# Optimization experiments

Measured on AMD Instinct MI355X. Metric: run time of the kernel, lower is better.

## Reference

```python
import jax, jax.numpy as jnp
import numpy as np

C = 64            # irrep multiplicity (64x0e + 64x1o)
N_BASIS = 8
N_SPECIES = 5
AVG_NEIGH = 16.0
CUTOFF = 5.0
N_PATHS = 5       # (0e*Y0->0e),(0e*Y1->1o),(1o*Y0->1o),(1o.Y1->0e),(1o x Y1->1)


def setup_inputs() -> dict:
    key = jax.random.key(0)
    ks = jax.random.split(key, 16)
    N, E = 20000, 320000
    def w(k, shape, fan_in):
        return jax.random.normal(k, shape, dtype=jnp.float32) / jnp.sqrt(jnp.float32(fan_in))
    return {
        "vectors": jax.random.normal(ks[0], (E, 3), dtype=jnp.float32),
        "node_feats": jax.random.normal(ks[1], (N, 4 * C), dtype=jnp.float32),
        "node_specie": jax.random.randint(ks[2], (N,), 0, N_SPECIES),
        "senders": jax.random.randint(ks[3], (E,), 0, N),
        "receivers": jax.random.randint(ks[4], (E,), 0, N),
        # linear_up (per-irrep channel mixing)
        "W0_up": w(ks[5], (C, C), C),
        "W1_up": w(ks[6], (C, C), C),
        # radial MLP: 8 -> 64 -> 64 -> 5*C
        "Wm1": w(ks[7], (N_BASIS, 64), N_BASIS),
        "Wm2": w(ks[8], (64, 64), 64),
        "Wm3": w(ks[9], (64, N_PATHS * C), 64),
        # skip_tp: species-indexed linear to 128x0e + 64x1o
        "Ws0": w(ks[10], (N_SPECIES, C, 2 * C), C),
        "Ws1": w(ks[11], (N_SPECIES, C, C), C),
        # linear_down: messages irreps -> 128x0e + 64x1o
        "Wd0": w(ks[12], (C, 2 * C), C),
        "Wd1": w(ks[13], (C, C), C),
    }


def reference(vectors, node_feats, node_specie, senders, receivers,
              W0_up, W1_up, Wm1, Wm2, Wm3, Ws0, Ws1, Wd0, Wd1):
    N = node_feats.shape[0]
    E = vectors.shape[0]
    x0 = node_feats[:, :C]                       # [N,C]   0e scalars
    x1 = node_feats[:, C:].reshape(N, C, 3)      # [N,C,3] 1o vectors

    # linear_up then gather by senders
    u0 = x0 @ W0_up
    u1 = jnp.einsum('nci,cd->ndi', x1, W1_up)
    m0 = u0[senders]                             # [E,C]
    m1 = u1[senders]                             # [E,C,3]

    # radial basis (bessel) and edge-weight MLP
    r = jnp.linalg.norm(vectors, axis=-1, keepdims=True)   # [E,1]
    safe_r = jnp.where(r == 0.0, 1.0, r)
    Y1 = vectors / safe_r                                  # [E,3] unit direction (l=1 SH)
    n = jnp.arange(1, N_BASIS + 1, dtype=vectors.dtype)
    basis = jnp.sqrt(2.0 / CUTOFF) * jnp.sin(n * jnp.pi * r / CUTOFF) / safe_r  # [E,8]
    h = jax.nn.silu(basis @ Wm1)
    h = jax.nn.silu(h @ Wm2)
    wmix = h @ Wm3                                         # [E, 5*C]
    wmix = jnp.where(r == 0.0, 0.0, wmix)                  # zero weights at zero-length edges
    w00, w01, w10, w11d, w11c = jnp.split(wmix, N_PATHS, axis=-1)  # each [E,C]

    # per-edge equivariant tensor product (LinearSHTP, l<=1 CG paths)
    dot = jnp.einsum('eci,ei->ec', m1, Y1)                 # 1o . Y1 -> scalar
    crs = jnp.cross(m1, Y1[:, None, :])                    # 1o x Y1 -> vector
    msg0 = w00 * m0 + w11d * dot                           # [E,C]
    msg1 = (w01 * m0)[..., None] * Y1[:, None, :] \
           + w10[..., None] * m1 + w11c[..., None] * crs   # [E,C,3]

    # scatter_sum to receivers, normalize by sqrt(avg_num_neighbors)
    inv = 1.0 / jnp.sqrt(jnp.float32(AVG_NEIGH))
    a0 = jax.ops.segment_sum(msg0, receivers, num_segments=N) * inv
    a1 = jax.ops.segment_sum(msg1.reshape(E, 3 * C), receivers, num_segments=N).reshape(N, C, 3) * inv

    # linear_down to 128x0e + 64x1o (extra 0e scalars are the gates)
    d0 = a0 @ Wd0                                          # [N,2C]
    d1 = jnp.einsum('nci,cd->ndi', a1, Wd1)                # [N,C,3]

    # skip_tp: species-indexed linear on original node features
    s0 = jnp.einsum('nc,ncd->nd', x0, Ws0[node_specie])    # [N,2C]
    s1 = jnp.einsum('nci,ncd->ndi', x1, Ws1[node_specie])  # [N,C,3]

    f0 = d0 + s0
    f1 = d1 + s1

    # gate: first C scalars -> even_act(silu); next C scalars gate the 1o vectors
    scalars = jax.nn.silu(f0[:, :C])
    gates = jax.nn.silu(f0[:, C:])
    vec = f1 * gates[..., None]
    return jnp.concatenate([scalars, vec.reshape(N, 3 * C)], axis=-1)  # [N, 4C]
```

## Files before the change

kernel.cpp:

```cpp
#include <hip/hip_runtime.h>
#include <hip/hip_bf16.h>

typedef __attribute__((ext_vector_type(8))) short short8;
typedef __attribute__((ext_vector_type(4))) float f32x4;

__device__ __forceinline__ unsigned bf16u(float x) {
    unsigned u = __float_as_uint(x);
    return (u + 0x7fffu + ((u >> 16) & 1u)) >> 16;
}
__device__ __forceinline__ short bf16s(float x) { return (short)bf16u(x); }

__global__ __launch_bounds__(256) void prep_kernel(
    const float* __restrict__ Wm1, const float* __restrict__ Wm2,
    const float* __restrict__ Wm3,
    const float* __restrict__ Wd0, const float* __restrict__ Ws0,
    const float* __restrict__ Wd1, const float* __restrict__ Ws1,
    short* __restrict__ W1B, short* __restrict__ Wm2B, short* __restrict__ W3B,
    short* __restrict__ WoB, int* __restrict__ cnt, int N)
{
    const int tid = blockIdx.x * 256 + threadIdx.x;
    const int nth = gridDim.x * 256;

    for (int i = tid; i < N * 16; i += nth) cnt[i] = 0;

    for (int idx = tid; idx < 52 * 64; idx += nth) {
        int l = idx & 63, f = idx >> 6;
        int g = l >> 4, c = l & 15;
        short8 v;
        if (f < 4) {
            #pragma unroll
            for (int i = 0; i < 8; ++i)
                v[i] = (g == 0) ? bf16s(Wm1[(size_t)i * 64 + f * 16 + c]) : (short)0;
            *(short8*)(W1B + (size_t)f * 512 + l * 8) = v;
        } else if (f < 12) {
            int f2 = f - 4, t = f2 >> 1, kh = f2 & 1;
            #pragma unroll
            for (int i = 0; i < 8; ++i)
                v[i] = bf16s(Wm2[(size_t)(kh * 32 + g * 8 + i) * 64 + t * 16 + c]);
            *(short8*)(Wm2B + (size_t)f2 * 512 + l * 8) = v;
        } else {
            int f3 = f - 12, t = f3 >> 1, kh = f3 & 1;
            #pragma unroll
            for (int i = 0; i < 8; ++i)
                v[i] = bf16s(Wm3[(size_t)(kh * 32 + g * 8 + i) * 320 + t * 16 + c]);
            *(short8*)(W3B + (size_t)f3 * 512 + l * 8) = v;
        }
    }

    for (int idx = tid; idx < 144 * 64; idx += nth) {
        int l = idx & 63, f = idx >> 6;
        int g = l >> 4, c = l & 15;
        short8 v;
        if (f < 16) {
            int t = f >> 1, kh = f & 1;
            #pragma unroll
            for (int i = 0; i < 8; ++i)
                v[i] = bf16s(Wd0[(size_t)(kh * 32 + g * 8 + i) * 128 + t * 16 + c]);
        } else if (f < 96) {
            int s = (f - 16) >> 4, r = (f - 16) & 15, t = r >> 1, kh = r & 1;
            #pragma unroll
            for (int i = 0; i < 8; ++i)
                v[i] = bf16s(Ws0[((size_t)s * 64 + kh * 32 + g * 8 + i) * 128 + t * 16 + c]);
        } else if (f < 104) {
            int r = f - 96, t = r >> 1, kh = r & 1;
            #pragma unroll
            for (int i = 0; i < 8; ++i)
                v[i] = bf16s(Wd1[(size_t)(kh * 32 + g * 8 + i) * 64 + t * 16 + c]);
        } else {
            int s = (f - 104) >> 3, r = (f - 104) & 7, t = r >> 1, kh = r & 1;
            #pragma unroll
            for (int i = 0; i < 8; ++i)
                v[i] = bf16s(Ws1[((size_t)s * 64 + kh * 32 + g * 8 + i) * 64 + t * 16 + c]);
        }
        *(short8*)(WoB + (size_t)f * 512 + l * 8) = v;
    }
}

__global__ __launch_bounds__(256) void rank_kernel(
    const int* __restrict__ receivers, int* __restrict__ cnt,
    int* __restrict__ rank, int E)
{
    int i = blockIdx.x * 256 + threadIdx.x;
    int stride = gridDim.x * 256;
    for (; i < E; i += stride)
        rank[i] = atomicAdd(&cnt[receivers[i] << 4], 1);
}

__global__ __launch_bounds__(256) void scan1_kernel(
    const int* __restrict__ cnt, int* __restrict__ offs,
    int* __restrict__ part, int N)
{
    __shared__ int a_[256], b_[256];
    const int b = blockIdx.x, t = threadIdx.x;
    const int base = b * 1024 + t * 4;
    int v[4];
    #pragma unroll
    for (int k = 0; k < 4; ++k)
        v[k] = (base + k < N) ? cnt[(size_t)(base + k) << 4] : 0;
    int sum = v[0] + v[1] + v[2] + v[3];
    a_[t] = sum;
    __syncthreads();
    int* src = a_; int* dst = b_;
    for (int off = 1; off < 256; off <<= 1) {
        dst[t] = src[t] + ((t >= off) ? src[t - off] : 0);
        __syncthreads();
        int* tmp = src; src = dst; dst = tmp;
    }
    int excl = src[t] - sum;
    if (t == 0) part[b] = src[255];
    int run = excl;
    #pragma unroll
    for (int k = 0; k < 4; ++k) {
        if (base + k < N) offs[base + k] = run;
        run += v[k];
    }
}

__global__ __launch_bounds__(256) void scan23_kernel(
    int* __restrict__ offs, const int* __restrict__ part, int nblk, int N)
{
    __shared__ int base_s, total_s;
    const int b = blockIdx.x, t = threadIdx.x;
    if (t == 0) {
        int s = 0, tot = 0;
        for (int i = 0; i < nblk; ++i) {
            if (i < b) s += part[i];
            tot += part[i];
        }
        base_s = s; total_s = tot;
    }
    __syncthreads();
    const int add = base_s;
    const int base = b * 1024 + t * 4;
    #pragma unroll
    for (int k = 0; k < 4; ++k) {
        int i = base + k;
        if (i < N) offs[i] += add;
    }
    if (b == 0 && t == 0) offs[N] = total_s;
}

__global__ __launch_bounds__(256) void fpnu_kernel(
    const float* __restrict__ vectors, const int* __restrict__ senders,
    const int* __restrict__ receivers, const int* __restrict__ offs,
    const int* __restrict__ rank,
    uint4* __restrict__ epackA, float4* __restrict__ epackB,
    const float* __restrict__ node_feats, const float* __restrict__ W0_up,
    const float* __restrict__ W1_up, uint2* __restrict__ ubf,
    short* __restrict__ xpk, int E, int N, int FPB)
{
    __shared__ float lnf[4][256];
    if (blockIdx.x < FPB) {
        int i = blockIdx.x * 256 + threadIdx.x;
        int stride = FPB * 256;
        for (; i < E; i += stride) {
            int pos = offs[receivers[i]] + rank[i];
            float vx = vectors[3 * (size_t)i + 0];
            float vy = vectors[3 * (size_t)i + 1];
            float vz = vectors[3 * (size_t)i + 2];
            float r = sqrtf(vx * vx + vy * vy + vz * vz);
            float ir = (r != 0.f) ? 1.f / r : 0.f;
            float ang = r * 0.6283185307179586f;
            float s1, c1;
            __sincosf(ang, &s1, &c1);
            float tc = 2.f * c1;
            float sb = s1, sp = 0.f;
            float coef = 0.6324555320336759f * ir;
            unsigned bw[4];
            #pragma unroll
            for (int h = 0; h < 4; ++h) {
                unsigned lo = bf16u(sb * coef);
                float nx = tc * sb - sp; sp = sb; sb = nx;
                unsigned hi = bf16u(sb * coef);
                nx = tc * sb - sp; sp = sb; sb = nx;
                bw[h] = lo | (hi << 16);
            }
            epackA[pos] = make_uint4(bw[0], bw[1], bw[2], bw[3]);
            epackB[pos] = make_float4(vx * ir, vy * ir, vz * ir,
                                      __int_as_float(senders[i]));
        }
    } else {
        const int wv = threadIdx.x >> 6;
        const int d  = threadIdx.x & 63;
        int nb = (blockIdx.x - FPB) * 4 + wv;
        if (nb >= N) return;

        float4 v4 = *(const float4*)(node_feats + (size_t)nb * 256 + d * 4);
        *(float4*)&lnf[wv][d * 4] = v4;

        float a0 = 0.f, ax = 0.f, ay = 0.f, az = 0.f;
        #pragma unroll 8
        for (int cc = 0; cc < 64; ++cc) {
            float w0 = W0_up[cc * 64 + d];
            float w1 = W1_up[cc * 64 + d];
            float x0v = lnf[wv][cc];
            float xxv = lnf[wv][64 + cc * 3 + 0];
            float xyv = lnf[wv][64 + cc * 3 + 1];
            float xzv = lnf[wv][64 + cc * 3 + 2];
            a0 += x0v * w0;
            ax += xxv * w1;
            ay += xyv * w1;
            az += xzv * w1;
        }
        ubf[(size_t)nb * 64 + d] = make_uint2(bf16u(a0) | (bf16u(ax) << 16),
                                              bf16u(ay) | (bf16u(az) << 16));
        short* xp = xpk + (size_t)nb * 256;
        xp[d]       = bf16s(lnf[wv][d]);
        xp[64 + d]  = bf16s(lnf[wv][64 + d * 3 + 0]);
        xp[128 + d] = bf16s(lnf[wv][64 + d * 3 + 1]);
        xp[192 + d] = bf16s(lnf[wv][64 + d * 3 + 2]);
    }
}

__global__ __launch_bounds__(256) void mlp_kernel(
    const uint4* __restrict__ epackA,
    const short* __restrict__ W1B, const short* __restrict__ Wm2B,
    const short* __restrict__ W3B, unsigned short* __restrict__ wmix,
    int P, int nwaves)
{
    __shared__ __align__(16) short ldsW3[40 * 512];
    __shared__ __align__(16) short ldsH[4][1024];

    {
        const short8* src = (const short8*)W3B;
        short8* dst = (short8*)ldsW3;
        for (int i = threadIdx.x; i < 2560; i += 256) dst[i] = src[i];
    }
    __syncthreads();

    const int lane = threadIdx.x & 63;
    const int wv   = threadIdx.x >> 6;
    const int gw   = blockIdx.x * 4 + wv;
    const int c = lane & 15, g = lane >> 4;
    const int nwin = (P + 15) >> 4;

    for (int w = gw; w < nwin; w += nwaves) {
        const int p0 = w << 4;

        short8 basisA = {0, 0, 0, 0, 0, 0, 0, 0};
        if (lane < 16) {
            uint4 ba = epackA[p0 + lane];
            union { uint4 u4v; short8 s8; } cv;
            cv.u4v = ba;
            basisA = cv.s8;
        }

        #pragma unroll
        for (int t = 0; t < 4; ++t) {
            f32x4 h = {0.f, 0.f, 0.f, 0.f};
            short8 bf = *(const short8*)(W1B + (size_t)t * 512 + lane * 8);
            h = __builtin_amdgcn_mfma_f32_16x16x32_bf16(basisA, bf, h, 0, 0, 0);
            #pragma unroll
            for (int i = 0; i < 4; ++i) {
                float x = h[i];
                float h1 = x / (1.f + __expf(-x));
                int row = 4 * g + i;
                ldsH[wv][row * 64 + ((16 * t + c) ^ ((row & 7) << 3))] = bf16s(h1);
            }
        }
        short8 h1f0 = *(const short8*)&ldsH[wv][c * 64 + ((g * 8) ^ ((c & 7) << 3))];
        short8 h1f1 = *(const short8*)&ldsH[wv][c * 64 + ((32 + g * 8) ^ ((c & 7) << 3))];

        #pragma unroll
        for (int t = 0; t < 4; ++t) {
            f32x4 h = {0.f, 0.f, 0.f, 0.f};
            short8 b0 = *(const short8*)(Wm2B + (size_t)(t * 2) * 512 + lane * 8);
            short8 b1 = *(const short8*)(Wm2B + (size_t)(t * 2 + 1) * 512 + lane * 8);
            h = __builtin_amdgcn_mfma_f32_16x16x32_bf16(h1f0, b0, h, 0, 0, 0);
            h = __builtin_amdgcn_mfma_f32_16x16x32_bf16(h1f1, b1, h, 0, 0, 0);
            #pragma unroll
            for (int i = 0; i < 4; ++i) {
                float x = h[i];
                float h2 = x / (1.f + __expf(-x));
                int row = 4 * g + i;
                ldsH[wv][row * 64 + ((16 * t + c) ^ ((row & 7) << 3))] = bf16s(h2);
            }
        }
        short8 h2f0 = *(const short8*)&ldsH[wv][c * 64 + ((g * 8) ^ ((c & 7) << 3))];
        short8 h2f1 = *(const short8*)&ldsH[wv][c * 64 + ((32 + g * 8) ^ ((c & 7) << 3))];

        size_t rowOfs[4];
        bool ok[4];
        #pragma unroll
        for (int i = 0; i < 4; ++i) {
            int row = p0 + 4 * g + i;
            ok[i] = (row < P);
            rowOfs[i] = (size_t)row * 320;
        }
        #pragma unroll
        for (int t = 0; t < 20; ++t) {
            f32x4 wq = {0.f, 0.f, 0.f, 0.f};
            short8 b0 = *(const short8*)(ldsW3 + (size_t)(t * 2) * 512 + lane * 8);
            short8 b1 = *(const short8*)(ldsW3 + (size_t)(t * 2 + 1) * 512 + lane * 8);
            wq = __builtin_amdgcn_mfma_f32_16x16x32_bf16(h2f0, b0, wq, 0, 0, 0);
            wq = __builtin_amdgcn_mfma_f32_16x16x32_bf16(h2f1, b1, wq, 0, 0, 0);
            const int col = (t >> 2) * 64 + (t & 3) * 16 + c;
            #pragma unroll
            for (int i = 0; i < 4; ++i)
                if (ok[i]) wmix[rowOfs[i] + col] = (unsigned short)bf16u(wq[i]);
        }
    }
}

__global__ __launch_bounds__(256) void gather_kernel(
    const float4* __restrict__ epackB, const int* __restrict__ offs,
    const uint2* __restrict__ ubf, const unsigned short* __restrict__ wmix,
    float* __restrict__ acc, int N)
{
    const int lane = threadIdx.x & 63;
    const int n = blockIdx.x * 4 + (threadIdx.x >> 6);
    if (n >= N) return;

    const int beg = offs[n], end = offs[n + 1];
    float a0 = 0.f, a1x = 0.f, a1y = 0.f, a1z = 0.f;

    #pragma unroll 2
    for (int pos = beg; pos < end; ++pos) {
        float4 mb = epackB[pos];
        int snd = __float_as_int(mb.w);
        uint2 mu = ubf[(size_t)snd * 64 + lane];
        const unsigned short* wr = wmix + (size_t)pos * 320;
        float w00  = __uint_as_float((unsigned)wr[lane]        << 16);
        float w01  = __uint_as_float((unsigned)wr[64 + lane]   << 16);
        float w10  = __uint_as_float((unsigned)wr[128 + lane]  << 16);
        float w11d = __uint_as_float((unsigned)wr[192 + lane]  << 16);
        float w11c = __uint_as_float((unsigned)wr[256 + lane]  << 16);
        float m0  = __uint_as_float(mu.x << 16);
        float m1x = __uint_as_float(mu.x & 0xffff0000u);
        float m1y = __uint_as_float(mu.y << 16);
        float m1z = __uint_as_float(mu.y & 0xffff0000u);

        float dotv = m1x * mb.x + m1y * mb.y + m1z * mb.z;
        a0 += w00 * m0 + w11d * dotv;
        float wm = w01 * m0;
        a1x += wm * mb.x + w10 * m1x + w11c * (m1y * mb.z - m1z * mb.y);
        a1y += wm * mb.y + w10 * m1y + w11c * (m1z * mb.x - m1x * mb.z);
        a1z += wm * mb.z + w10 * m1z + w11c * (m1x * mb.y - m1y * mb.x);
    }

    float* ar = acc + (size_t)n * 256;
    ar[lane]       = a0;
    ar[64 + lane]  = a1x;
    ar[128 + lane] = a1y;
    ar[192 + lane] = a1z;
}

__global__ __launch_bounds__(256) void edge_kernel(
    const uint4* __restrict__ epackA, const float4* __restrict__ epackB,
    const int* __restrict__ offs, const uint2* __restrict__ ubf,
    const short* __restrict__ W1B, const short* __restrict__ Wm2B,
    const short* __restrict__ W3B, float* __restrict__ acc,
    int N, int nwaves)
{
    __shared__ __align__(16) short ldsW3[40 * 512];
    __shared__ __align__(16) short ldsH[4][1024];
    __shared__ __align__(16) float ldsMeta[4][16][4];

    {
        const short8* src = (const short8*)W3B;
        short8* dst = (short8*)ldsW3;
        for (int i = threadIdx.x; i < 2560; i += 256) dst[i] = src[i];
    }
    __syncthreads();

    const int lane = threadIdx.x & 63;
    const int wv   = threadIdx.x >> 6;
    const int gw   = blockIdx.x * 4 + wv;
    const int c = lane & 15, g = lane >> 4;

    for (int n = gw; n < N; n += nwaves) {
        float a0q[4]  = {0.f, 0.f, 0.f, 0.f};
        float a1xq[4] = {0.f, 0.f, 0.f, 0.f};
        float a1yq[4] = {0.f, 0.f, 0.f, 0.f};
        float a1zq[4] = {0.f, 0.f, 0.f, 0.f};
        const int beg = offs[n], end = offs[n + 1];

        for (int p0 = beg; p0 < end; p0 += 16) {
            const int m = end - p0;
            short8 basisA = {0, 0, 0, 0, 0, 0, 0, 0};
            if (lane < 16) {
                uint4 ba = epackA[p0 + lane];
                float4 mb = epackB[p0 + lane];
                if (lane >= m) {
                    ba = make_uint4(0u, 0u, 0u, 0u);
                    mb = make_float4(0.f, 0.f, 0.f, __int_as_float(0));
                }
                union { uint4 u4v; short8 s8; } cv;
                cv.u4v = ba;
                basisA = cv.s8;
                *(float4*)&ldsMeta[wv][lane][0] = mb;
            }
            float Yx[4], Yy[4], Yz[4];
            int snd[4];
            #pragma unroll
            for (int i = 0; i < 4; ++i) {
                float4 mt = *(const float4*)&ldsMeta[wv][4 * g + i][0];
                Yx[i] = mt.x; Yy[i] = mt.y; Yz[i] = mt.z;
                snd[i] = __float_as_int(mt.w);
            }

#define PFETCH(Q, MV)                                                       \
            _Pragma("unroll")                                               \
            for (int i = 0; i < 4; ++i)                                     \
                MV[i] = ubf[(size_t)snd[i] * 64 + 16 * (Q) + c];

#define COMPQ(Q, MV)                                                        \
        {                                                                   \
            float M0[4], M1X[4], M1Y[4], M1Z[4];                            \
            _Pragma("unroll")                                               \
            for (int i = 0; i < 4; ++i) {                                   \
                M0[i]  = __uint_as_float(MV[i].x << 16);                    \
                M1X[i] = __uint_as_float(MV[i].x & 0xffff0000u);            \
                M1Y[i] = __uint_as_float(MV[i].y << 16);                    \
                M1Z[i] = __uint_as_float(MV[i].y & 0xffff0000u);            \
            }                                                               \
            _Pragma("unroll")                                               \
            for (int p = 0; p < 5; ++p) {                                   \
                const int t = 4 * p + (Q);                                  \
                f32x4 w = {0.f, 0.f, 0.f, 0.f};                             \
                short8 b0 = *(const short8*)(ldsW3 + (size_t)(t * 2) * 512 + lane * 8);     \
                short8 b1 = *(const short8*)(ldsW3 + (size_t)(t * 2 + 1) * 512 + lane * 8); \
                w = __builtin_amdgcn_mfma_f32_16x16x32_bf16(h2f0, b0, w, 0, 0, 0);          \
                w = __builtin_amdgcn_mfma_f32_16x16x32_bf16(h2f1, b1, w, 0, 0, 0);          \
                _Pragma("unroll")                                           \
                for (int i = 0; i < 4; ++i) {                               \
                    float wv_ = w[i];                                       \
                    if (p == 0) {                                           \
                        a0q[Q] += wv_ * M0[i];                              \
                    } else if (p == 1) {                                    \
                        float tt = wv_ * M0[i];                             \
                        a1xq[Q] += tt * Yx[i];                              \
                        a1yq[Q] += tt * Yy[i];                              \
                        a1zq[Q] += tt * Yz[i];                              \
                    } else if (p == 2) {                                    \
                        a1xq[Q] += wv_ * M1X[i];                            \
                        a1yq[Q] += wv_ * M1Y[i];                            \
                        a1zq[Q] += wv_ * M1Z[i];                            \
                    } else if (p == 3) {                                    \
                        a0q[Q] += wv_ * (M1X[i] * Yx[i] + M1Y[i] * Yy[i] + M1Z[i] * Yz[i]); \
                    } else {                                                \
                        a1xq[Q] += wv_ * (M1Y[i] * Yz[i] - M1Z[i] * Yy[i]); \
                        a1yq[Q] += wv_ * (M1Z[i] * Yx[i] - M1X[i] * Yz[i]); \
                        a1zq[Q] += wv_ * (M1X[i] * Yy[i] - M1Y[i] * Yx[i]); \
                    }                                                       \
                }                                                           \
            }                                                               \
        }

            uint2 mA[4], mB[4];
            PFETCH(0, mA);
            PFETCH(1, mB);
            __builtin_amdgcn_sched_barrier(0);

            #pragma unroll
            for (int t = 0; t < 4; ++t) {
                f32x4 h = {0.f, 0.f, 0.f, 0.f};
                short8 bf = *(const short8*)(W1B + (size_t)t * 512 + lane * 8);
                h = __builtin_amdgcn_mfma_f32_16x16x32_bf16(basisA, bf, h, 0, 0, 0);
                #pragma unroll
                for (int i = 0; i < 4; ++i) {
                    float x = h[i];
                    float h1 = x / (1.f + __expf(-x));
                    int row = 4 * g + i;
                    ldsH[wv][row * 64 + ((16 * t + c) ^ ((row & 7) << 3))] = bf16s(h1);
                }
            }
            short8 h1f0 = *(const short8*)&ldsH[wv][c * 64 + ((g * 8) ^ ((c & 7) << 3))];
            short8 h1f1 = *(const short8*)&ldsH[wv][c * 64 + ((32 + g * 8) ^ ((c & 7) << 3))];

            #pragma unroll
            for (int t = 0; t < 4; ++t) {
                f32x4 h = {0.f, 0.f, 0.f, 0.f};
                short8 b0 = *(const short8*)(Wm2B + (size_t)(t * 2) * 512 + lane * 8);
                short8 b1 = *(const short8*)(Wm2B + (size_t)(t * 2 + 1) * 512 + lane * 8);
                h = __builtin_amdgcn_mfma_f32_16x16x32_bf16(h1f0, b0, h, 0, 0, 0);
                h = __builtin_amdgcn_mfma_f32_16x16x32_bf16(h1f1, b1, h, 0, 0, 0);
                #pragma unroll
                for (int i = 0; i < 4; ++i) {
                    float x = h[i];
                    float h2 = x / (1.f + __expf(-x));
                    int row = 4 * g + i;
                    ldsH[wv][row * 64 + ((16 * t + c) ^ ((row & 7) << 3))] = bf16s(h2);
                }
            }
            short8 h2f0 = *(const short8*)&ldsH[wv][c * 64 + ((g * 8) ^ ((c & 7) << 3))];
            short8 h2f1 = *(const short8*)&ldsH[wv][c * 64 + ((32 + g * 8) ^ ((c & 7) << 3))];

            COMPQ(0, mA);
            __builtin_amdgcn_sched_barrier(0);
            PFETCH(2, mA);
            COMPQ(1, mB);
            __builtin_amdgcn_sched_barrier(0);
            PFETCH(3, mB);
            COMPQ(2, mA);
            __builtin_amdgcn_sched_barrier(0);
            COMPQ(3, mB);
#undef PFETCH
#undef COMPQ
        }

        #pragma unroll
        for (int q = 0; q < 4; ++q) {
            a0q[q]  += __shfl_xor(a0q[q], 16);  a0q[q]  += __shfl_xor(a0q[q], 32);
            a1xq[q] += __shfl_xor(a1xq[q], 16); a1xq[q] += __shfl_xor(a1xq[q], 32);
            a1yq[q] += __shfl_xor(a1yq[q], 16); a1yq[q] += __shfl_xor(a1yq[q], 32);
            a1zq[q] += __shfl_xor(a1zq[q], 16); a1zq[q] += __shfl_xor(a1zq[q], 32);
        }
        if (lane < 16) {
            float* ar = acc + (size_t)n * 256;
            #pragma unroll
            for (int q = 0; q < 4; ++q) {
                ar[16 * q + lane]       = a0q[q];
                ar[64 + 16 * q + lane]  = a1xq[q];
                ar[128 + 16 * q + lane] = a1yq[q];
                ar[192 + 16 * q + lane] = a1zq[q];
            }
        }
    }
}

__global__ __launch_bounds__(256) void node_out_kernel(
    const float* __restrict__ acc, const short* __restrict__ xpk,
    const int* __restrict__ node_specie, const short* __restrict__ WoB,
    float* __restrict__ out, int N)
{
    __shared__ float ldsOut[4][16][256];
    const int lane = threadIdx.x & 63;
    const int wv   = threadIdx.x >> 6;
    const int c = lane & 15, g = lane >> 4;
    const int n0 = (blockIdx.x * 4 + wv) * 16;
    if (n0 >= N) return;

    const int nc = min(n0 + c, N - 1);
    const int sp_c = node_specie[nc];
    const short8 z8 = {0, 0, 0, 0, 0, 0, 0, 0};

    short8 x0f[2], a0hi[2], a0lo[2];
    #pragma unroll
    for (int kh = 0; kh < 2; ++kh) {
        x0f[kh] = *(const short8*)&xpk[(size_t)nc * 256 + kh * 32 + g * 8];
        const float* ap = acc + (size_t)nc * 256 + kh * 32 + g * 8;
        #pragma unroll
        for (int i = 0; i < 8; ++i) {
            float v = 0.25f * ap[i];
            unsigned h = bf16u(v);
            a0hi[kh][i] = (short)h;
            a0lo[kh][i] = (short)bf16u(v - __uint_as_float(h << 16));
        }
    }

    f32x4 w0[8];
    #pragma unroll
    for (int t = 0; t < 8; ++t) w0[t] = (f32x4){0.f, 0.f, 0.f, 0.f};
    #pragma unroll
    for (int t = 0; t < 8; ++t)
        #pragma unroll
        for (int kh = 0; kh < 2; ++kh) {
            short8 b = *(const short8*)(WoB + (size_t)(t * 2 + kh) * 512 + lane * 8);
            w0[t] = __builtin_amdgcn_mfma_f32_16x16x32_bf16(a0hi[kh], b, w0[t], 0, 0, 0);
            w0[t] = __builtin_amdgcn_mfma_f32_16x16x32_bf16(a0lo[kh], b, w0[t], 0, 0, 0);
        }
    #pragma unroll
    for (int s = 0; s < 5; ++s) {
        if (!__any(sp_c == s)) continue;
        short8 mk0 = (sp_c == s) ? x0f[0] : z8;
        short8 mk1 = (sp_c == s) ? x0f[1] : z8;
        #pragma unroll
        for (int t = 0; t < 8; ++t) {
            short8 b0 = *(const short8*)(WoB + (size_t)(16 + s * 16 + t * 2) * 512 + lane * 8);
            short8 b1 = *(const short8*)(WoB + (size_t)(16 + s * 16 + t * 2 + 1) * 512 + lane * 8);
            w0[t] = __builtin_amdgcn_mfma_f32_16x16x32_bf16(mk0, b0, w0[t], 0, 0, 0);
            w0[t] = __builtin_amdgcn_mfma_f32_16x16x32_bf16(mk1, b1, w0[t], 0, 0, 0);
        }
    }
    float gate[4][4];
    #pragma unroll
    for (int t = 0; t < 8; ++t)
        #pragma unroll
        for (int i = 0; i < 4; ++i) {
            float x = w0[t][i];
            float sv = x / (1.f + __expf(-x));
            if (t < 4) ldsOut[wv][4 * g + i][16 * t + c] = sv;
            else       gate[t - 4][i] = sv;
        }

    short8 x1f[3][2], a1hi[3][2], a1lo[3][2];
    #pragma unroll
    for (int j = 0; j < 3; ++j)
        #pragma unroll
        for (int kh = 0; kh < 2; ++kh) {
            x1f[j][kh] = *(const short8*)&xpk[(size_t)nc * 256 + (1 + j) * 64 + kh * 32 + g * 8];
            const float* ap = acc + (size_t)nc * 256 + 64 + 64 * j + kh * 32 + g * 8;
            #pragma unroll
            for (int i = 0; i < 8; ++i) {
                float v = 0.25f * ap[i];
                unsigned h = bf16u(v);
                a1hi[j][kh][i] = (short)h;
                a1lo[j][kh][i] = (short)bf16u(v - __uint_as_float(h << 16));
            }
        }

    f32x4 w1[3][4];
    #pragma unroll
    for (int j = 0; j < 3; ++j)
        #pragma unroll
        for (int t = 0; t < 4; ++t) w1[j][t] = (f32x4){0.f, 0.f, 0.f, 0.f};
    #pragma unroll
    for (int t = 0; t < 4; ++t)
        #pragma unroll
        for (int kh = 0; kh < 2; ++kh) {
            short8 b = *(const short8*)(WoB + (size_t)(96 + t * 2 + kh) * 512 + lane * 8);
            #pragma unroll
            for (int j = 0; j < 3; ++j) {
                w1[j][t] = __builtin_amdgcn_mfma_f32_16x16x32_bf16(a1hi[j][kh], b, w1[j][t], 0, 0, 0);
                w1[j][t] = __builtin_amdgcn_mfma_f32_16x16x32_bf16(a1lo[j][kh], b, w1[j][t], 0, 0, 0);
            }
        }
    #pragma unroll
    for (int s = 0; s < 5; ++s) {
        if (!__any(sp_c == s)) continue;
        short8 m1[3][2];
        #pragma unroll
        for (int j = 0; j < 3; ++j) {
            m1[j][0] = (sp_c == s) ? x1f[j][0] : z8;
            m1[j][1] = (sp_c == s) ? x1f[j][1] : z8;
        }
        #pragma unroll
        for (int t = 0; t < 4; ++t)
            #pragma unroll
            for (int kh = 0; kh < 2; ++kh) {
                short8 b = *(const short8*)(WoB + (size_t)(104 + s * 8 + t * 2 + kh) * 512 + lane * 8);
                #pragma unroll
                for (int j = 0; j < 3; ++j)
                    w1[j][t] = __builtin_amdgcn_mfma_f32_16x16x32_bf16(m1[j][kh], b, w1[j][t], 0, 0, 0);
            }
    }
    #pragma unroll
    for (int j = 0; j < 3; ++j)
        #pragma unroll
        for (int t = 0; t < 4; ++t)
            #pragma unroll
            for (int i = 0; i < 4; ++i)
                ldsOut[wv][4 * g + i][64 + (16 * t + c) * 3 + j] = w1[j][t][i] * gate[t][i];

    #pragma unroll 4
    for (int r = 0; r < 16; ++r) {
        int nn = n0 + r;
        if (nn < N)
            *(float4*)&out[(size_t)nn * 256 + lane * 4] =
                *(const float4*)&ldsOut[wv][r][lane * 4];
    }
}

extern "C" void kernel_launch(void* const* d_in, const int* in_sizes, int n_in,
                              void* d_out, int out_size, void* d_ws, size_t ws_size,
                              hipStream_t stream) {
    const float* vectors     = (const float*)d_in[0];
    const float* node_feats  = (const float*)d_in[1];
    const int*   node_specie = (const int*)d_in[2];
    const int*   senders     = (const int*)d_in[3];
    const int*   receivers   = (const int*)d_in[4];
    const float* W0_up       = (const float*)d_in[5];
    const float* W1_up       = (const float*)d_in[6];
    const float* Wm1         = (const float*)d_in[7];
    const float* Wm2         = (const float*)d_in[8];
    const float* Wm3         = (const float*)d_in[9];
    const float* Ws0         = (const float*)d_in[10];
    const float* Ws1         = (const float*)d_in[11];
    const float* Wd0         = (const float*)d_in[12];
    const float* Wd1         = (const float*)d_in[13];
    float* out = (float*)d_out;

    int E = in_sizes[0] / 3;
    int N = in_sizes[1] / 256;
    int nblk = (N + 1023) / 1024;

    char* wp = (char*)d_ws;
    uint2* ubf     = (uint2*)wp;                wp += (size_t)N * 64 * 8;
    float* acc     = (float*)wp;                wp += (size_t)N * 256 * 4;
    short* xpk     = (short*)wp;                wp += (size_t)N * 256 * 2;
    uint4* epackA  = (uint4*)wp;                wp += (size_t)(E + 16) * 16;
    float4* epackB = (float4*)wp;               wp += (size_t)(E + 16) * 16;
    unsigned short* wmix = (unsigned short*)wp;
    size_t wmix_bytes = (size_t)(E + 16) * 320 * 2;
    size_t base_used = (size_t)(wp - (char*)d_ws);
    size_t other_bytes = (4 + 8 + 40 + 144) * 512 * 2
                       + (size_t)N * 16 * 4
                       + (size_t)(N + 1) * 4
                       + (size_t)E * 4
                       + (size_t)(nblk + 1) * 4 + 256;
    bool use_split = (base_used + wmix_bytes + other_bytes) <= ws_size;
    if (use_split) wp += wmix_bytes;

    short* W1B    = (short*)wp;                 wp += 4 * 512 * 2;
    short* Wm2B   = (short*)wp;                 wp += 8 * 512 * 2;
    short* W3B    = (short*)wp;                 wp += 40 * 512 * 2;
    short* WoB    = (short*)wp;                 wp += 144 * 512 * 2;
    int*   cnt    = (int*)wp;                   wp += (size_t)N * 16 * 4;
    int*   offs   = (int*)wp;                   wp += (size_t)(N + 1) * 4;
    int*   rank   = (int*)wp;                   wp += (size_t)E * 4;
    int*   part   = (int*)wp;                   wp += (size_t)(nblk + 1) * 4;

    prep_kernel<<<80, 256, 0, stream>>>(
        Wm1, Wm2, Wm3, Wd0, Ws0, Wd1, Ws1, W1B, Wm2B, W3B, WoB, cnt, N);
    rank_kernel<<<1024, 256, 0, stream>>>(receivers, cnt, rank, E);
    scan1_kernel<<<nblk, 256, 0, stream>>>(cnt, offs, part, N);
    scan23_kernel<<<nblk, 256, 0, stream>>>(offs, part, nblk, N);
    const int FPB = 1024;
    fpnu_kernel<<<FPB + (N + 3) / 4, 256, 0, stream>>>(
        vectors, senders, receivers, offs, rank, epackA, epackB,
        node_feats, W0_up, W1_up, ubf, xpk, E, N, FPB);

    if (use_split) {
        mlp_kernel<<<768, 256, 0, stream>>>(
            epackA, W1B, Wm2B, W3B, wmix, E, 768 * 4);
        gather_kernel<<<(N + 3) / 4, 256, 0, stream>>>(
            epackB, offs, ubf, wmix, acc, N);
    } else {
        edge_kernel<<<512, 256, 0, stream>>>(
            epackA, epackB, offs, ubf, W1B, Wm2B, W3B, acc, N, 512 * 4);
    }

    int ngroups = (N + 15) / 16;
    node_out_kernel<<<(ngroups + 3) / 4, 256, 0, stream>>>(
        acc, xpk, node_specie, WoB, out, N);
}
```

Before: 195.7 us.

## Store edge weights in MFMA-native tiled layout with vectorized 8-byte stores and loads

The weight-MLP kernel now writes each wave's 16-edge by 320-column result tile directly in the MFMA fragment order, as one 4-element bf16 vector store per lane per tile, with no per-row bounds checks or scattered 2-byte stores. The gather kernel reads that tiled layout in groups of four edges, loading five 8-byte vectors per group instead of five 2-byte loads per edge, and masks edges outside the node's range. This trades scattered narrow global writes and reads for wide coalesced ones. It requires the wmix buffer to be padded to a multiple of 16 edges, and boundary edges at group edges are loaded and then discarded.

```diff
diff --git a/kernel.cpp b/kernel.cpp
--- a/kernel.cpp
+++ b/kernel.cpp
@@ -3,6 +3,7 @@
 
 typedef __attribute__((ext_vector_type(8))) short short8;
 typedef __attribute__((ext_vector_type(4))) float f32x4;
+typedef __attribute__((ext_vector_type(4))) unsigned short us4v;
 
 __device__ __forceinline__ unsigned bf16u(float x) {
     unsigned u = __float_as_uint(x);
@@ -279,14 +280,7 @@
         short8 h2f0 = *(const short8*)&ldsH[wv][c * 64 + ((g * 8) ^ ((c & 7) << 3))];
         short8 h2f1 = *(const short8*)&ldsH[wv][c * 64 + ((32 + g * 8) ^ ((c & 7) << 3))];
 
-        size_t rowOfs[4];
-        bool ok[4];
-        #pragma unroll
-        for (int i = 0; i < 4; ++i) {
-            int row = p0 + 4 * g + i;
-            ok[i] = (row < P);
-            rowOfs[i] = (size_t)row * 320;
-        }
+        unsigned short* wbase = wmix + (size_t)w * 5120 + lane * 4;
         #pragma unroll
         for (int t = 0; t < 20; ++t) {
             f32x4 wq = {0.f, 0.f, 0.f, 0.f};
@@ -294,10 +288,10 @@
             short8 b1 = *(const short8*)(ldsW3 + (size_t)(t * 2 + 1) * 512 + lane * 8);
             wq = __builtin_amdgcn_mfma_f32_16x16x32_bf16(h2f0, b0, wq, 0, 0, 0);
             wq = __builtin_amdgcn_mfma_f32_16x16x32_bf16(h2f1, b1, wq, 0, 0, 0);
-            const int col = (t >> 2) * 64 + (t & 3) * 16 + c;
-            #pragma unroll
-            for (int i = 0; i < 4; ++i)
-                if (ok[i]) wmix[rowOfs[i] + col] = (unsigned short)bf16u(wq[i]);
+            us4v st;
+            #pragma unroll
+            for (int i = 0; i < 4; ++i) st[i] = (unsigned short)bf16u(wq[i]);
+            *(us4v*)(wbase + t * 256) = st;
         }
     }
 }
@@ -310,32 +304,45 @@
     const int lane = threadIdx.x & 63;
     const int n = blockIdx.x * 4 + (threadIdx.x >> 6);
     if (n >= N) return;
+    const int q = lane >> 4, c = lane & 15;
 
     const int beg = offs[n], end = offs[n + 1];
     float a0 = 0.f, a1x = 0.f, a1y = 0.f, a1z = 0.f;
 
-    #pragma unroll 2
-    for (int pos = beg; pos < end; ++pos) {
-        float4 mb = epackB[pos];
-        int snd = __float_as_int(mb.w);
-        uint2 mu = ubf[(size_t)snd * 64 + lane];
-        const unsigned short* wr = wmix + (size_t)pos * 320;
-        float w00  = __uint_as_float((unsigned)wr[lane]        << 16);
-        float w01  = __uint_as_float((unsigned)wr[64 + lane]   << 16);
-        float w10  = __uint_as_float((unsigned)wr[128 + lane]  << 16);
-        float w11d = __uint_as_float((unsigned)wr[192 + lane]  << 16);
-        float w11c = __uint_as_float((unsigned)wr[256 + lane]  << 16);
-        float m0  = __uint_as_float(mu.x << 16);
-        float m1x = __uint_as_float(mu.x & 0xffff0000u);
-        float m1y = __uint_as_float(mu.y << 16);
-        float m1z = __uint_as_float(mu.y & 0xffff0000u);
-
-        float dotv = m1x * mb.x + m1y * mb.y + m1z * mb.z;
-        a0 += w00 * m0 + w11d * dotv;
-        float wm = w01 * m0;
-        a1x += wm * mb.x + w10 * m1x + w11c * (m1y * mb.z - m1z * mb.y);
-        a1y += wm * mb.y + w10 * m1y + w11c * (m1z * mb.x - m1x * mb.z);
-        a1z += wm * mb.z + w10 * m1z + w11c * (m1x * mb.y - m1y * mb.x);
+    for (int base = beg & ~3; base < end; base += 4) {
+        const unsigned short* wn = wmix
+            + (size_t)(base >> 4) * 5120
+            + (q << 8) + (((base & 15) >> 2) << 6) + (c << 2);
+        us4v wp0 = *(const us4v*)(wn);
+        us4v wp1 = *(const us4v*)(wn + 1024);
+        us4v wp2 = *(const us4v*)(wn + 2048);
+        us4v wp3 = *(const us4v*)(wn + 3072);
+        us4v wp4 = *(const us4v*)(wn + 4096);
+
+        #pragma unroll
+        for (int i = 0; i < 4; ++i) {
+            int pos = base + i;
+            bool valid = (pos >= beg) && (pos < end);
+            float4 mb = epackB[pos];
+            int snd = valid ? __float_as_int(mb.w) : 0;
+            uint2 mu = ubf[(size_t)snd * 64 + lane];
+            float w00  = valid ? __uint_as_float((unsigned)wp0[i] << 16) : 0.f;
+            float w01  = valid ? __uint_as_float((unsigned)wp1[i] << 16) : 0.f;
+            float w10  = valid ? __uint_as_float((unsigned)wp2[i] << 16) : 0.f;
+            float w11d = valid ? __uint_as_float((unsigned)wp3[i] << 16) : 0.f;
+            float w11c = valid ? __uint_as_float((unsigned)wp4[i] << 16) : 0.f;
+            float m0  = __uint_as_float(mu.x << 16);
+            float m1x = __uint_as_float(mu.x & 0xffff0000u);
+            float m1y = __uint_as_float(mu.y << 16);
+            float m1z = __uint_as_float(mu.y & 0xffff0000u);
+
+            float dotv = m1x * mb.x + m1y * mb.y + m1z * mb.z;
+            a0 += w00 * m0 + w11d * dotv;
+            float wm = w01 * m0;
+            a1x += wm * mb.x + w10 * m1x + w11c * (m1y * mb.z - m1z * mb.y);
+            a1y += wm * mb.y + w10 * m1y + w11c * (m1z * mb.x - m1x * mb.z);
+            a1z += wm * mb.z + w10 * m1z + w11c * (m1x * mb.y - m1y * mb.x);
+        }
     }
 
     float* ar = acc + (size_t)n * 256;
```

Result: slower. 205.1 us (+4.8%).
